# Kernel tuning notes

Measured on AMD Instinct MI355X. Metric: run time of the kernel, lower is better.

## Reference

```python
import jax, jax.numpy as jnp
import numpy as np

N_NODES = 100000
N_EDGES = 3200000
DIM = 16


def setup_inputs() -> dict:
    key = jax.random.key(0)
    k1, k2, k3, k4 = jax.random.split(key, 4)
    state_input = jax.random.normal(k1, (N_NODES, DIM), dtype=jnp.float32)
    row = jax.random.randint(k2, (N_EDGES,), 0, N_NODES, dtype=jnp.int32)
    col = jax.random.randint(k3, (N_EDGES,), 0, N_NODES, dtype=jnp.int32)
    edge_weights = jax.random.uniform(k4, (N_EDGES,), dtype=jnp.float32)
    return {"state_input": state_input, "row": row, "col": col,
            "edge_weights": edge_weights}


def reference(state_input, row, col, edge_weights):
    # f_eq: per-dim self dynamics, f(x) = -x  -> [N, dim]
    self_diff = -state_input

    # gather pair endpoints: x_1 = state[col], x_2 = state[row]
    # g_eq: sin(x_2 - x_1) per dim (Kuramoto-style coupling) -> [E, dim]
    neighbor_processed = jnp.sin(state_input[row] - state_input[col])

    # weight by edge weight and scatter-sum into destination nodes (col)
    aggregated_sum = jax.ops.segment_sum(
        neighbor_processed * edge_weights[:, None], col,
        num_segments=state_input.shape[0])  # [N, dim]

    # s_eq: elementwise tanh on aggregated sum
    interact_diff = jnp.tanh(aggregated_sum)

    return (self_diff + interact_diff,
            (state_input, self_diff),
            (aggregated_sum, interact_diff))
```

## Files before the change

kernel.cpp:

```cpp
#include <hip/hip_runtime.h>
#include <hip/hip_fp16.h>
#include <math.h>

#define N_NODES 100000
#define N_EDGES 3200000
#define DIM 16
#define NSZ (N_NODES * DIM)

#define NPB 128
#define NBUCK 782
#define NBLK 512
#define EPB 6256
#define CAP 4864
#define PRK 5

typedef float nvec4 __attribute__((ext_vector_type(4)));

__global__ __launch_bounds__(512)
void prep(const float* __restrict__ state, const int* __restrict__ col,
          __half* __restrict__ hs, float* __restrict__ out,
          unsigned* __restrict__ tbl, int* __restrict__ totals) {
    __shared__ int hcnt[NBUCK];
    int t = threadIdx.x, blk = blockIdx.x;
    for (int j = t; j < NBUCK; j += 512) hcnt[j] = 0;
    int gid = blk * 512 + t, gsz = NBLK * 512;
    for (int i = gid; i < NSZ / 4; i += gsz) {
        nvec4 v = __builtin_nontemporal_load(&((const nvec4*)state)[i]);
        union { __half2 h[2]; float2 f; } u;
        u.h[0] = __floats2half2_rn(v.x, v.y);
        u.h[1] = __floats2half2_rn(v.z, v.w);
        ((float2*)hs)[i] = u.f;
        __builtin_nontemporal_store(v, &((nvec4*)(out + 1 * (size_t)NSZ))[i]);
        nvec4 nv = {-v.x, -v.y, -v.z, -v.w};
        __builtin_nontemporal_store(nv, &((nvec4*)(out + 2 * (size_t)NSZ))[i]);
    }
    __syncthreads();
    int e0 = blk * EPB;
    int eN = e0 + EPB; if (eN > N_EDGES) eN = N_EDGES;
    int nch = (eN - e0) >> 2;
    const int4* c4p = (const int4*)(col + e0);
    for (int i = t; i < nch; i += 512) {
        int4 c = c4p[i];
        atomicAdd(&hcnt[c.x >> 7], 1);
        atomicAdd(&hcnt[c.y >> 7], 1);
        atomicAdd(&hcnt[c.z >> 7], 1);
        atomicAdd(&hcnt[c.w >> 7], 1);
    }
    __syncthreads();
    for (int j = t; j < NBUCK; j += 512) {
        int c = hcnt[j];
        tbl[(size_t)j * NBLK + blk] = (unsigned)c;
        if (c) atomicAdd(&totals[j], c);
    }
}

__global__ __launch_bounds__(512)
void scan_off(const int* __restrict__ totals, int* __restrict__ off) {
    __shared__ int wsum[8];
    int t = threadIdx.x;
    int i0 = 2 * t, i1 = 2 * t + 1;
    int v0 = (i0 < NBUCK) ? totals[i0] : 0;
    int v1 = (i1 < NBUCK) ? totals[i1] : 0;
    int p = v0 + v1, ps = p;
    #pragma unroll
    for (int d = 1; d < 64; d <<= 1) {
        int u = __shfl_up(ps, d, 64);
        if ((t & 63) >= d) ps += u;
    }
    if ((t & 63) == 63) wsum[t >> 6] = ps;
    __syncthreads();
    int wid = t >> 6, wbase = 0;
    #pragma unroll
    for (int k = 0; k < 8; ++k) wbase += (k < wid) ? wsum[k] : 0;
    int ex = wbase + ps - p;
    if (i0 <= NBUCK) off[i0] = ex;
    if (i1 <= NBUCK) off[i1] = ex + v0;
}

__global__ __launch_bounds__(512)
void base_scan(unsigned* __restrict__ tbl, const int* __restrict__ off) {
    __shared__ int wsum[8];
    int b = blockIdx.x, t = threadIdx.x;
    int v = (int)tbl[(size_t)b * NBLK + t];
    int ps = v;
    #pragma unroll
    for (int d = 1; d < 64; d <<= 1) {
        int u = __shfl_up(ps, d, 64);
        if ((t & 63) >= d) ps += u;
    }
    if ((t & 63) == 63) wsum[t >> 6] = ps;
    __syncthreads();
    int wid = t >> 6, wbase = 0;
    #pragma unroll
    for (int k = 0; k < 8; ++k) wbase += (k < wid) ? wsum[k] : 0;
    tbl[(size_t)b * NBLK + t] = (unsigned)(off[b] + wbase + ps - v);
}

__global__ __launch_bounds__(512)
void sort_write(const int* __restrict__ row, const int* __restrict__ col,
                const float* __restrict__ w, const unsigned* __restrict__ tbl,
                const int* __restrict__ off,
                unsigned long long* __restrict__ packed) {
    __shared__ unsigned long long sbuf[EPB];
    __shared__ int cur[NBUCK];
    __shared__ int diff[NBUCK];
    __shared__ int wsum[8];
    int t = threadIdx.x, blk = blockIdx.x;
    int e0 = blk * EPB;
    int eN = e0 + EPB; if (eN > N_EDGES) eN = N_EDGES;
    int cnt = eN - e0;

    for (int j = t; j < NBUCK; j += 512) {
        int b0 = (int)tbl[(size_t)j * NBLK + blk];
        int b1 = (blk == NBLK - 1) ? off[j + 1]
                                   : (int)tbl[(size_t)j * NBLK + blk + 1];
        diff[j] = b0;
        cur[j] = b1 - b0;
    }
    __syncthreads();
    {
        int i0 = 2 * t, i1 = 2 * t + 1;
        int v0 = (i0 < NBUCK) ? cur[i0] : 0;
        int v1 = (i1 < NBUCK) ? cur[i1] : 0;
        int p = v0 + v1, ps = p;
        #pragma unroll
        for (int d = 1; d < 64; d <<= 1) {
            int u = __shfl_up(ps, d, 64);
            if ((t & 63) >= d) ps += u;
        }
        if ((t & 63) == 63) wsum[t >> 6] = ps;
        __syncthreads();
        int wid = t >> 6, wbase = 0;
        #pragma unroll
        for (int k = 0; k < 8; ++k) wbase += (k < wid) ? wsum[k] : 0;
        int ex = wbase + ps - p;
        if (i0 < NBUCK) { diff[i0] -= ex;      cur[i0] = ex; }
        if (i1 < NBUCK) { diff[i1] -= ex + v0; cur[i1] = ex + v0; }
    }
    __syncthreads();
    {
        int nch = cnt >> 2;
        const int4*   c4p = (const int4*)(col + e0);
        const int4*   r4p = (const int4*)(row + e0);
        const float4* w4p = (const float4*)(w + e0);
        for (int i = t; i < nch; i += 512) {
            int4 c = c4p[i]; int4 r = r4p[i]; float4 ww = w4p[i];
            int pos;
            pos = atomicAdd(&cur[c.x >> 7], 1);
            sbuf[pos] = ((unsigned long long)(unsigned)c.x << 47)
                      | ((unsigned long long)(unsigned)r.x << 30)
                      | (unsigned long long)(__float_as_uint(ww.x) >> 2);
            pos = atomicAdd(&cur[c.y >> 7], 1);
            sbuf[pos] = ((unsigned long long)(unsigned)c.y << 47)
                      | ((unsigned long long)(unsigned)r.y << 30)
                      | (unsigned long long)(__float_as_uint(ww.y) >> 2);
            pos = atomicAdd(&cur[c.z >> 7], 1);
            sbuf[pos] = ((unsigned long long)(unsigned)c.z << 47)
                      | ((unsigned long long)(unsigned)r.z << 30)
                      | (unsigned long long)(__float_as_uint(ww.z) >> 2);
            pos = atomicAdd(&cur[c.w >> 7], 1);
            sbuf[pos] = ((unsigned long long)(unsigned)c.w << 47)
                      | ((unsigned long long)(unsigned)r.w << 30)
                      | (unsigned long long)(__float_as_uint(ww.w) >> 2);
        }
    }
    __syncthreads();
    for (int i = t; i < cnt; i += 512) {
        unsigned long long pv = sbuf[i];
        int b = (int)(pv >> 54);
        __builtin_nontemporal_store(pv, &packed[diff[b] + i]);
    }
}

__global__ __launch_bounds__(1024, 8)
void aggregate(const float* __restrict__ state, const __half2* __restrict__ hs2,
               const int* __restrict__ off,
               const unsigned long long* __restrict__ packed,
               float* __restrict__ out) {
    __shared__ unsigned long long sbuf[CAP];
    __shared__ int s_cnt[NPB], s_start[NPB], s_cur[NPB];
    __shared__ int s_wsum;
    int b = blockIdx.x, t = threadIdx.x;
    int q = t & 3, sub = (t >> 2) & 1, g = t >> 3;
    int beg = off[b], end = off[b + 1];
    int n = b * NPB + g;
    bool valid = (n < N_NODES);
    float4 xx = valid ? ((const float4*)state)[n * 4 + q]
                      : make_float4(0.f, 0.f, 0.f, 0.f);
    float4 acc = {0.f, 0.f, 0.f, 0.f};
    const uint2* hsu = (const uint2*)hs2;

    for (int tbeg = beg; tbeg < end; tbeg += CAP) {
        int tend = tbeg + CAP; if (tend > end) tend = end;
        if (t < NPB) s_cnt[t] = 0;
        __syncthreads();

        unsigned long long pr[PRK];
        #pragma unroll
        for (int k = 0; k < PRK; ++k) {
            int e = tbeg + t + k * 1024;
            if (e < tend) {
                pr[k] = __builtin_nontemporal_load(&packed[e]);
                atomicAdd(&s_cnt[(unsigned)(pr[k] >> 47) & 127u], 1);
            }
        }
        __syncthreads();

        {
            int v = 0, ps = 0;
            if (t < NPB) {
                v = s_cnt[t]; ps = v;
                #pragma unroll
                for (int d = 1; d < 64; d <<= 1) {
                    int u = __shfl_up(ps, d, 64);
                    if ((t & 63) >= d) ps += u;
                }
            }
            if (t == 63) s_wsum = ps;
            __syncthreads();
            if (t < NPB) {
                int ex = ps - v + ((t >= 64) ? s_wsum : 0);
                s_start[t] = ex;
                s_cur[t] = ex;
            }
        }
        __syncthreads();

        #pragma unroll
        for (int k = 0; k < PRK; ++k) {
            int e = tbeg + t + k * 1024;
            if (e < tend) {
                int cl = (int)((pr[k] >> 47) & 127u);
                int pos = atomicAdd(&s_cur[cl], 1);
                sbuf[pos] = pr[k];
            }
        }
        __syncthreads();

        {
            int es = s_start[g], ee = s_cur[g];
            int e = es + sub;
            for (; e + 6 < ee; e += 8) {
                unsigned long long p0 = sbuf[e];
                unsigned long long p1 = sbuf[e + 2];
                unsigned long long p2 = sbuf[e + 4];
                unsigned long long p3 = sbuf[e + 6];
                uint2 h0 = hsu[(unsigned)((p0 >> 30) & 0x1FFFFu) * 4u + q];
                uint2 h1 = hsu[(unsigned)((p1 >> 30) & 0x1FFFFu) * 4u + q];
                uint2 h2 = hsu[(unsigned)((p2 >> 30) & 0x1FFFFu) * 4u + q];
                uint2 h3 = hsu[(unsigned)((p3 >> 30) & 0x1FFFFu) * 4u + q];
                #pragma unroll
                for (int j = 0; j < 4; ++j) {
                    unsigned long long p = (j == 0) ? p0 : (j == 1) ? p1
                                         : (j == 2) ? p2 : p3;
                    uint2 hb = (j == 0) ? h0 : (j == 1) ? h1
                             : (j == 2) ? h2 : h3;
                    float we = __uint_as_float(((unsigned)p & 0x3FFFFFFFu) << 2);
                    float2 lo = __half22float2(*(const __half2*)&hb.x);
                    float2 hi = __half22float2(*(const __half2*)&hb.y);
                    acc.x += __sinf(lo.x - xx.x) * we;
                    acc.y += __sinf(lo.y - xx.y) * we;
                    acc.z += __sinf(hi.x - xx.z) * we;
                    acc.w += __sinf(hi.y - xx.w) * we;
                }
            }
            for (; e < ee; e += 2) {
                unsigned long long p = sbuf[e];
                uint2 hb = hsu[(unsigned)((p >> 30) & 0x1FFFFu) * 4u + q];
                float we = __uint_as_float(((unsigned)p & 0x3FFFFFFFu) << 2);
                float2 lo = __half22float2(*(const __half2*)&hb.x);
                float2 hi = __half22float2(*(const __half2*)&hb.y);
                acc.x += __sinf(lo.x - xx.x) * we;
                acc.y += __sinf(lo.y - xx.y) * we;
                acc.z += __sinf(hi.x - xx.z) * we;
                acc.w += __sinf(hi.y - xx.w) * we;
            }
        }
        __syncthreads();
    }

    acc.x += __shfl_xor(acc.x, 4, 64); acc.y += __shfl_xor(acc.y, 4, 64);
    acc.z += __shfl_xor(acc.z, 4, 64); acc.w += __shfl_xor(acc.w, 4, 64);

    if (valid && sub == 0) {
        float4 th = make_float4(tanhf(acc.x), tanhf(acc.y),
                                tanhf(acc.z), tanhf(acc.w));
        int gdx = n * 4 + q;
        nvec4 v0 = {th.x - xx.x, th.y - xx.y, th.z - xx.z, th.w - xx.w};
        nvec4 v3 = {acc.x, acc.y, acc.z, acc.w};
        nvec4 v4 = {th.x, th.y, th.z, th.w};
        __builtin_nontemporal_store(v0, &((nvec4*)(out + 0 * (size_t)NSZ))[gdx]);
        __builtin_nontemporal_store(v3, &((nvec4*)(out + 3 * (size_t)NSZ))[gdx]);
        __builtin_nontemporal_store(v4, &((nvec4*)(out + 4 * (size_t)NSZ))[gdx]);
    }
}

__global__ __launch_bounds__(256)
void edge_kernel(const float* __restrict__ state, const int* __restrict__ row,
                 const int* __restrict__ col, const float* __restrict__ w,
                 float* __restrict__ agg) {
    int idx = blockIdx.x * blockDim.x + threadIdx.x;
    if (idx >= N_EDGES * 4) return;
    int e = idx >> 2, qq = idx & 3;
    int r = row[e], c = col[e];
    float we = w[e];
    const float4 xr = ((const float4*)state)[r * 4 + qq];
    const float4 xcv = ((const float4*)state)[c * 4 + qq];
    float* dst = agg + c * DIM + qq * 4;
    atomicAdd(dst + 0, sinf(xr.x - xcv.x) * we);
    atomicAdd(dst + 1, sinf(xr.y - xcv.y) * we);
    atomicAdd(dst + 2, sinf(xr.z - xcv.z) * we);
    atomicAdd(dst + 3, sinf(xr.w - xcv.w) * we);
}

__global__ __launch_bounds__(256)
void node_kernel(const float* __restrict__ state, const float* __restrict__ agg,
                 float* __restrict__ out) {
    int idx = blockIdx.x * blockDim.x + threadIdx.x;
    if (idx >= N_NODES * 4) return;
    float4 x = ((const float4*)state)[idx];
    float4 a = ((const float4*)agg)[idx];
    float4 tv = make_float4(tanhf(a.x), tanhf(a.y), tanhf(a.z), tanhf(a.w));
    ((float4*)(out + 0 * NSZ))[idx] = make_float4(tv.x - x.x, tv.y - x.y,
                                                  tv.z - x.z, tv.w - x.w);
    ((float4*)(out + 1 * NSZ))[idx] = x;
    ((float4*)(out + 2 * NSZ))[idx] = make_float4(-x.x, -x.y, -x.z, -x.w);
    ((float4*)(out + 4 * NSZ))[idx] = tv;
}

extern "C" void kernel_launch(void* const* d_in, const int* in_sizes, int n_in,
                              void* d_out, int out_size, void* d_ws, size_t ws_size,
                              hipStream_t stream) {
    const float* state = (const float*)d_in[0];
    const int*   row   = (const int*)d_in[1];
    const int*   col   = (const int*)d_in[2];
    const float* w     = (const float*)d_in[3];
    float* out = (float*)d_out;

    size_t packed_off = 0;
    size_t hs_off     = packed_off + (size_t)N_EDGES * 8;
    size_t tbl_off    = hs_off + (size_t)NSZ * 2;
    size_t tot_off    = tbl_off + (size_t)NBUCK * NBLK * 4;
    size_t off_off    = tot_off + ((size_t)NBUCK * 4 + 15) / 16 * 16;
    size_t needed     = off_off + (size_t)(NBUCK + 2) * 4;

    if (ws_size >= needed) {
        unsigned long long* packed =
            (unsigned long long*)((char*)d_ws + packed_off);
        __half* hs    = (__half*)((char*)d_ws + hs_off);
        unsigned* tbl = (unsigned*)((char*)d_ws + tbl_off);
        int* totals   = (int*)((char*)d_ws + tot_off);
        int* off      = (int*)((char*)d_ws + off_off);

        (void)hipMemsetAsync(totals, 0, (size_t)NBUCK * sizeof(int), stream);
        prep<<<NBLK, 512, 0, stream>>>(state, col, hs, out, tbl, totals);
        scan_off<<<1, 512, 0, stream>>>(totals, off);
        base_scan<<<NBUCK, 512, 0, stream>>>(tbl, off);
        sort_write<<<NBLK, 512, 0, stream>>>(row, col, w, tbl, off, packed);
        aggregate<<<NBUCK, 1024, 0, stream>>>(
            state, (const __half2*)hs, off, packed, out);
    } else {
        float* agg = out + 3 * NSZ;
        (void)hipMemsetAsync(agg, 0, NSZ * sizeof(float), stream);
        edge_kernel<<<(N_EDGES * 4 + 255) / 256, 256, 0, stream>>>(
            state, row, col, w, agg);
        node_kernel<<<(N_NODES * 4 + 255) / 256, 256, 0, stream>>>(
            state, agg, out);
    }
}
```

Measured before the change: 174.6 us.

## Fold offset scan into prep via last-block ticket; persistent aggregate grid with work queue

The single-block scan_off kernel is removed. The last prep block to finish, detected with an atomic ticket after a threadfence, now computes the bucket offsets, which saves one kernel launch. The aggregate kernel becomes persistent: 512 blocks take bucket indices dynamically from an atomic counter instead of launching one block per bucket, which is meant to reduce tail imbalance and block launch overhead. The cost is extra atomics, a serialized tail in prep, and loop-carried synchronization in aggregate.

New measurement: 286.2 us. 63.9% more time.

```diff
diff --git a/kernel.cpp b/kernel.cpp
--- a/kernel.cpp
+++ b/kernel.cpp
@@ -13,14 +13,18 @@
 #define EPB 6256
 #define CAP 4864
 #define PRK 5
+#define AGG_GRID 512
 
 typedef float nvec4 __attribute__((ext_vector_type(4)));
 
 __global__ __launch_bounds__(512)
 void prep(const float* __restrict__ state, const int* __restrict__ col,
           __half* __restrict__ hs, float* __restrict__ out,
-          unsigned* __restrict__ tbl, int* __restrict__ totals) {
+          unsigned* __restrict__ tbl, int* __restrict__ totals,
+          int* __restrict__ ticket, int* __restrict__ off) {
     __shared__ int hcnt[NBUCK];
+    __shared__ int s_last;
+    __shared__ int wsum[8];
     int t = threadIdx.x, blk = blockIdx.x;
     for (int j = t; j < NBUCK; j += 512) hcnt[j] = 0;
     int gid = blk * 512 + t, gsz = NBLK * 512;
@@ -52,29 +56,29 @@
         tbl[(size_t)j * NBLK + blk] = (unsigned)c;
         if (c) atomicAdd(&totals[j], c);
     }
-}
-
-__global__ __launch_bounds__(512)
-void scan_off(const int* __restrict__ totals, int* __restrict__ off) {
-    __shared__ int wsum[8];
-    int t = threadIdx.x;
-    int i0 = 2 * t, i1 = 2 * t + 1;
-    int v0 = (i0 < NBUCK) ? totals[i0] : 0;
-    int v1 = (i1 < NBUCK) ? totals[i1] : 0;
-    int p = v0 + v1, ps = p;
-    #pragma unroll
-    for (int d = 1; d < 64; d <<= 1) {
-        int u = __shfl_up(ps, d, 64);
-        if ((t & 63) >= d) ps += u;
-    }
-    if ((t & 63) == 63) wsum[t >> 6] = ps;
-    __syncthreads();
-    int wid = t >> 6, wbase = 0;
-    #pragma unroll
-    for (int k = 0; k < 8; ++k) wbase += (k < wid) ? wsum[k] : 0;
-    int ex = wbase + ps - p;
-    if (i0 <= NBUCK) off[i0] = ex;
-    if (i1 <= NBUCK) off[i1] = ex + v0;
+    __threadfence();
+    if (t == 0) s_last = (atomicAdd(ticket, 1) == NBLK - 1) ? 1 : 0;
+    __syncthreads();
+    if (s_last) {
+        __threadfence();
+        int i0 = 2 * t, i1 = 2 * t + 1;
+        int v0 = (i0 < NBUCK) ? totals[i0] : 0;
+        int v1 = (i1 < NBUCK) ? totals[i1] : 0;
+        int p = v0 + v1, ps = p;
+        #pragma unroll
+        for (int d = 1; d < 64; d <<= 1) {
+            int u = __shfl_up(ps, d, 64);
+            if ((t & 63) >= d) ps += u;
+        }
+        if ((t & 63) == 63) wsum[t >> 6] = ps;
+        __syncthreads();
+        int wid = t >> 6, wbase = 0;
+        #pragma unroll
+        for (int k = 0; k < 8; ++k) wbase += (k < wid) ? wsum[k] : 0;
+        int ex = wbase + ps - p;
+        if (i0 <= NBUCK) off[i0] = ex;
+        if (i1 <= NBUCK) off[i1] = ex + v0;
+    }
 }
 
 __global__ __launch_bounds__(512)
@@ -176,85 +180,100 @@
 void aggregate(const float* __restrict__ state, const __half2* __restrict__ hs2,
                const int* __restrict__ off,
                const unsigned long long* __restrict__ packed,
-               float* __restrict__ out) {
+               int* __restrict__ qctr, float* __restrict__ out) {
     __shared__ unsigned long long sbuf[CAP];
     __shared__ int s_cnt[NPB], s_start[NPB], s_cur[NPB];
-    __shared__ int s_wsum;
-    int b = blockIdx.x, t = threadIdx.x;
+    __shared__ int s_wsum, s_nb;
+    int t = threadIdx.x;
     int q = t & 3, sub = (t >> 2) & 1, g = t >> 3;
-    int beg = off[b], end = off[b + 1];
-    int n = b * NPB + g;
-    bool valid = (n < N_NODES);
-    float4 xx = valid ? ((const float4*)state)[n * 4 + q]
-                      : make_float4(0.f, 0.f, 0.f, 0.f);
-    float4 acc = {0.f, 0.f, 0.f, 0.f};
     const uint2* hsu = (const uint2*)hs2;
 
-    for (int tbeg = beg; tbeg < end; tbeg += CAP) {
-        int tend = tbeg + CAP; if (tend > end) tend = end;
-        if (t < NPB) s_cnt[t] = 0;
-        __syncthreads();
-
-        unsigned long long pr[PRK];
-        #pragma unroll
-        for (int k = 0; k < PRK; ++k) {
-            int e = tbeg + t + k * 1024;
-            if (e < tend) {
-                pr[k] = __builtin_nontemporal_load(&packed[e]);
-                atomicAdd(&s_cnt[(unsigned)(pr[k] >> 47) & 127u], 1);
+    int nb = blockIdx.x;
+    while (nb < NBUCK) {
+        int beg = off[nb], end = off[nb + 1];
+        int n = nb * NPB + g;
+        bool valid = (n < N_NODES);
+        float4 xx = valid ? ((const float4*)state)[n * 4 + q]
+                          : make_float4(0.f, 0.f, 0.f, 0.f);
+        float4 acc = {0.f, 0.f, 0.f, 0.f};
+
+        for (int tbeg = beg; tbeg < end; tbeg += CAP) {
+            int tend = tbeg + CAP; if (tend > end) tend = end;
+            if (t < NPB) s_cnt[t] = 0;
+            __syncthreads();
+
+            unsigned long long pr[PRK];
+            #pragma unroll
+            for (int k = 0; k < PRK; ++k) {
+                int e = tbeg + t + k * 1024;
+                if (e < tend) {
+                    pr[k] = __builtin_nontemporal_load(&packed[e]);
+                    atomicAdd(&s_cnt[(unsigned)(pr[k] >> 47) & 127u], 1);
+                }
             }
-        }
-        __syncthreads();
-
-        {
-            int v = 0, ps = 0;
-            if (t < NPB) {
-                v = s_cnt[t]; ps = v;
-                #pragma unroll
-                for (int d = 1; d < 64; d <<= 1) {
-                    int u = __shfl_up(ps, d, 64);
-                    if ((t & 63) >= d) ps += u;
+            __syncthreads();
+
+            {
+                int v = 0, ps = 0;
+                if (t < NPB) {
+                    v = s_cnt[t]; ps = v;
+                    #pragma unroll
+                    for (int d = 1; d < 64; d <<= 1) {
+                        int u = __shfl_up(ps, d, 64);
+                        if ((t & 63) >= d) ps += u;
+                    }
+                }
+                if (t == 63) s_wsum = ps;
+                __syncthreads();
+                if (t < NPB) {
+                    int ex = ps - v + ((t >= 64) ? s_wsum : 0);
+                    s_start[t] = ex;
+                    s_cur[t] = ex;
                 }
             }
-            if (t == 63) s_wsum = ps;
-            __syncthreads();
-            if (t < NPB) {
-                int ex = ps - v + ((t >= 64) ? s_wsum : 0);
-                s_start[t] = ex;
-                s_cur[t] = ex;
+            __syncthreads();
+
+            #pragma unroll
+            for (int k = 0; k < PRK; ++k) {
+                int e = tbeg + t + k * 1024;
+                if (e < tend) {
+                    int cl = (int)((pr[k] >> 47) & 127u);
+                    int pos = atomicAdd(&s_cur[cl], 1);
+                    sbuf[pos] = pr[k];
+                }
             }
-        }
-        __syncthreads();
-
-        #pragma unroll
-        for (int k = 0; k < PRK; ++k) {
-            int e = tbeg + t + k * 1024;
-            if (e < tend) {
-                int cl = (int)((pr[k] >> 47) & 127u);
-                int pos = atomicAdd(&s_cur[cl], 1);
-                sbuf[pos] = pr[k];
-            }
-        }
-        __syncthreads();
-
-        {
-            int es = s_start[g], ee = s_cur[g];
-            int e = es + sub;
-            for (; e + 6 < ee; e += 8) {
-                unsigned long long p0 = sbuf[e];
-                unsigned long long p1 = sbuf[e + 2];
-                unsigned long long p2 = sbuf[e + 4];
-                unsigned long long p3 = sbuf[e + 6];
-                uint2 h0 = hsu[(unsigned)((p0 >> 30) & 0x1FFFFu) * 4u + q];
-                uint2 h1 = hsu[(unsigned)((p1 >> 30) & 0x1FFFFu) * 4u + q];
-                uint2 h2 = hsu[(unsigned)((p2 >> 30) & 0x1FFFFu) * 4u + q];
-                uint2 h3 = hsu[(unsigned)((p3 >> 30) & 0x1FFFFu) * 4u + q];
-                #pragma unroll
-                for (int j = 0; j < 4; ++j) {
-                    unsigned long long p = (j == 0) ? p0 : (j == 1) ? p1
-                                         : (j == 2) ? p2 : p3;
-                    uint2 hb = (j == 0) ? h0 : (j == 1) ? h1
-                             : (j == 2) ? h2 : h3;
+            __syncthreads();
+
+            {
+                int es = s_start[g], ee = s_cur[g];
+                int e = es + sub;
+                for (; e + 6 < ee; e += 8) {
+                    unsigned long long p0 = sbuf[e];
+                    unsigned long long p1 = sbuf[e + 2];
+                    unsigned long long p2 = sbuf[e + 4];
+                    unsigned long long p3 = sbuf[e + 6];
+                    uint2 h0 = hsu[(unsigned)((p0 >> 30) & 0x1FFFFu) * 4u + q];
+                    uint2 h1 = hsu[(unsigned)((p1 >> 30) & 0x1FFFFu) * 4u + q];
+                    uint2 h2 = hsu[(unsigned)((p2 >> 30) & 0x1FFFFu) * 4u + q];
+                    uint2 h3 = hsu[(unsigned)((p3 >> 30) & 0x1FFFFu) * 4u + q];
+                    #pragma unroll
+                    for (int j = 0; j < 4; ++j) {
+                        unsigned long long p = (j == 0) ? p0 : (j == 1) ? p1
+                                             : (j == 2) ? p2 : p3;
+                        uint2 hb = (j == 0) ? h0 : (j == 1) ? h1
+                                 : (j == 2) ? h2 : h3;
+                        float we = __uint_as_float(((unsigned)p & 0x3FFFFFFFu) << 2);
+                        float2 lo = __half22float2(*(const __half2*)&hb.x);
+                        float2 hi = __half22float2(*(const __half2*)&hb.y);
+                        acc.x += __sinf(lo.x - xx.x) * we;
+                        acc.y += __sinf(lo.y - xx.y) * we;
+                        acc.z += __sinf(hi.x - xx.z) * we;
+                        acc.w += __sinf(hi.y - xx.w) * we;
+                    }
+                }
+                for (; e < ee; e += 2) {
+                    unsigned long long p = sbuf[e];
+                    uint2 hb = hsu[(unsigned)((p >> 30) & 0x1FFFFu) * 4u + q];
                     float we = __uint_as_float(((unsigned)p & 0x3FFFFFFFu) << 2);
                     float2 lo = __half22float2(*(const __half2*)&hb.x);
                     float2 hi = __half22float2(*(const __half2*)&hb.y);
@@ -264,34 +283,27 @@
                     acc.w += __sinf(hi.y - xx.w) * we;
                 }
             }
-            for (; e < ee; e += 2) {
-                unsigned long long p = sbuf[e];
-                uint2 hb = hsu[(unsigned)((p >> 30) & 0x1FFFFu) * 4u + q];
-                float we = __uint_as_float(((unsigned)p & 0x3FFFFFFFu) << 2);
-                float2 lo = __half22float2(*(const __half2*)&hb.x);
-                float2 hi = __half22float2(*(const __half2*)&hb.y);
-                acc.x += __sinf(lo.x - xx.x) * we;
-                acc.y += __sinf(lo.y - xx.y) * we;
-                acc.z += __sinf(hi.x - xx.z) * we;
-                acc.w += __sinf(hi.y - xx.w) * we;
-            }
+            __syncthreads();
+        }
+
+        acc.x += __shfl_xor(acc.x, 4, 64); acc.y += __shfl_xor(acc.y, 4, 64);
+        acc.z += __shfl_xor(acc.z, 4, 64); acc.w += __shfl_xor(acc.w, 4, 64);
+
+        if (valid && sub == 0) {
+            float4 th = make_float4(tanhf(acc.x), tanhf(acc.y),
+                                    tanhf(acc.z), tanhf(acc.w));
+            int gdx = n * 4 + q;
+            nvec4 v0 = {th.x - xx.x, th.y - xx.y, th.z - xx.z, th.w - xx.w};
+            nvec4 v3 = {acc.x, acc.y, acc.z, acc.w};
+            nvec4 v4 = {th.x, th.y, th.z, th.w};
+            __builtin_nontemporal_store(v0, &((nvec4*)(out + 0 * (size_t)NSZ))[gdx]);
+            __builtin_nontemporal_store(v3, &((nvec4*)(out + 3 * (size_t)NSZ))[gdx]);
+            __builtin_nontemporal_store(v4, &((nvec4*)(out + 4 * (size_t)NSZ))[gdx]);
         }
         __syncthreads();
-    }
-
-    acc.x += __shfl_xor(acc.x, 4, 64); acc.y += __shfl_xor(acc.y, 4, 64);
-    acc.z += __shfl_xor(acc.z, 4, 64); acc.w += __shfl_xor(acc.w, 4, 64);
-
-    if (valid && sub == 0) {
-        float4 th = make_float4(tanhf(acc.x), tanhf(acc.y),
-                                tanhf(acc.z), tanhf(acc.w));
-        int gdx = n * 4 + q;
-        nvec4 v0 = {th.x - xx.x, th.y - xx.y, th.z - xx.z, th.w - xx.w};
-        nvec4 v3 = {acc.x, acc.y, acc.z, acc.w};
-        nvec4 v4 = {th.x, th.y, th.z, th.w};
-        __builtin_nontemporal_store(v0, &((nvec4*)(out + 0 * (size_t)NSZ))[gdx]);
-        __builtin_nontemporal_store(v3, &((nvec4*)(out + 3 * (size_t)NSZ))[gdx]);
-        __builtin_nontemporal_store(v4, &((nvec4*)(out + 4 * (size_t)NSZ))[gdx]);
+        if (t == 0) s_nb = AGG_GRID + atomicAdd(qctr, 1);
+        __syncthreads();
+        nb = s_nb;
     }
 }
 
@@ -341,7 +353,7 @@
     size_t hs_off     = packed_off + (size_t)N_EDGES * 8;
     size_t tbl_off    = hs_off + (size_t)NSZ * 2;
     size_t tot_off    = tbl_off + (size_t)NBUCK * NBLK * 4;
-    size_t off_off    = tot_off + ((size_t)NBUCK * 4 + 15) / 16 * 16;
+    size_t off_off    = tot_off + ((size_t)(NBUCK + 2) * 4 + 15) / 16 * 16;
     size_t needed     = off_off + (size_t)(NBUCK + 2) * 4;
 
     if (ws_size >= needed) {
@@ -350,15 +362,18 @@
         __half* hs    = (__half*)((char*)d_ws + hs_off);
         unsigned* tbl = (unsigned*)((char*)d_ws + tbl_off);
         int* totals   = (int*)((char*)d_ws + tot_off);
+        int* ticket   = totals + NBUCK;
+        int* qctr     = totals + NBUCK + 1;
         int* off      = (int*)((char*)d_ws + off_off);
 
-        (void)hipMemsetAsync(totals, 0, (size_t)NBUCK * sizeof(int), stream);
-        prep<<<NBLK, 512, 0, stream>>>(state, col, hs, out, tbl, totals);
-        scan_off<<<1, 512, 0, stream>>>(totals, off);
+        (void)hipMemsetAsync(totals, 0, (size_t)(NBUCK + 2) * sizeof(int),
+                             stream);
+        prep<<<NBLK, 512, 0, stream>>>(state, col, hs, out, tbl, totals,
+                                       ticket, off);
         base_scan<<<NBUCK, 512, 0, stream>>>(tbl, off);
         sort_write<<<NBLK, 512, 0, stream>>>(row, col, w, tbl, off, packed);
-        aggregate<<<NBUCK, 1024, 0, stream>>>(
-            state, (const __half2*)hs, off, packed, out);
+        aggregate<<<AGG_GRID, 1024, 0, stream>>>(
+            state, (const __half2*)hs, off, packed, qctr, out);
     } else {
         float* agg = out + 3 * NSZ;
         (void)hipMemsetAsync(agg, 0, NSZ * sizeof(float), stream);
```
